# Performance work log

Measured on AMD Instinct MI355X. Metric: run time of the kernel, lower is better.

The kernel has to match this reference:

```python
import jax, jax.numpy as jnp
import numpy as np

DIM = 768
NUM_HEADS = 12
HEAD_DIM = DIM // NUM_HEADS
SCALE = HEAD_DIM ** -0.5


def setup_inputs() -> dict:
    key = jax.random.key(0)
    ks = jax.random.split(key, 6)
    B, N, C = 4, 2048, DIM
    x = jax.random.normal(ks[0], (B, N, C), dtype=jnp.float32)
    qkv_weight = jax.random.normal(ks[1], (3 * C, C), dtype=jnp.float32) * (C ** -0.5)
    q_bias = jax.random.normal(ks[2], (C,), dtype=jnp.float32) * 0.02
    v_bias = jax.random.normal(ks[3], (C,), dtype=jnp.float32) * 0.02
    proj_weight = jax.random.normal(ks[4], (C, C), dtype=jnp.float32) * (C ** -0.5)
    proj_bias = jax.random.normal(ks[5], (C,), dtype=jnp.float32) * 0.02
    return {"x": x, "qkv_weight": qkv_weight, "q_bias": q_bias,
            "v_bias": v_bias, "proj_weight": proj_weight, "proj_bias": proj_bias}


def reference(x, qkv_weight, q_bias, v_bias, proj_weight, proj_bias):
    B, N, C = x.shape
    # bias = concat(q_bias, zeros_like(v_bias), v_bias)
    bias = jnp.concatenate([q_bias, jnp.zeros_like(v_bias), v_bias])
    qkv = x @ qkv_weight.T + bias                      # [B, N, 3C]
    qkv = qkv.reshape(B, N, 3, NUM_HEADS, HEAD_DIM)
    q, k, v = jnp.moveaxis(qkv, 2, 0)                  # each [B, N, H, hd]
    q = jnp.transpose(q, (0, 2, 1, 3)) * SCALE         # [B, H, N, hd]
    k = jnp.transpose(k, (0, 2, 1, 3))
    v = jnp.transpose(v, (0, 2, 1, 3))
    attn = jax.nn.softmax(jnp.einsum('bhqd,bhkd->bhqk', q, k), axis=-1)
    out = jnp.einsum('bhqk,bhkd->bhqd', attn, v)       # [B, H, N, hd]
    out = jnp.transpose(out, (0, 2, 1, 3)).reshape(B, N, C)
    return out @ proj_weight.T + proj_bias
```

## Files before the change

kernel.cpp:

```cpp
#include <hip/hip_runtime.h>
#include <cstdint>
#include <cstddef>

typedef _Float16 f16;
typedef _Float16 f16x8 __attribute__((ext_vector_type(8)));
typedef _Float16 f16x4 __attribute__((ext_vector_type(4)));
typedef __fp16 h16x2 __attribute__((ext_vector_type(2)));
typedef float f32x4 __attribute__((ext_vector_type(4)));

#define DIM 768
#define NHEAD 12
#define HD 64
#define BATCH 4
#define SEQ 2048
#define MROWS (BATCH*SEQ)
#define C3 (3*DIM)
#define NBH (BATCH*NHEAD)

__device__ __forceinline__ f32x4 mfma32(f16x8 a, f16x8 b, f32x4 c) {
  return __builtin_amdgcn_mfma_f32_16x16x32_f16(a, b, c, 0, 0, 0);
}
__device__ __forceinline__ f32x4 mfma16(f16x4 a, f16x4 b, f32x4 c) {
  return __builtin_amdgcn_mfma_f32_16x16x16f16(a, b, c, 0, 0, 0);
}

__device__ __forceinline__ void gl2lds16(const void* g, void* l) {
  __builtin_amdgcn_global_load_lds(
      (const __attribute__((address_space(1))) void*)g,
      (__attribute__((address_space(3))) void*)l, 16, 0, 0);
}

__global__ __launch_bounds__(256) void k_convert(
    const float* __restrict__ x, const float* __restrict__ wqkv,
    const float* __restrict__ wproj,
    f16* __restrict__ xh, f16* __restrict__ wqh, f16* __restrict__ wph)
{
  const int NX = MROWS*DIM/4, NW = C3*DIM/4;
  int i = blockIdx.x * 256 + threadIdx.x;
  const float4* src; f16* dst; int idx;
  if (i < NX)         { src = (const float4*)x;     dst = xh;  idx = i; }
  else if (i < NX+NW) { src = (const float4*)wqkv;  dst = wqh; idx = i - NX; }
  else                { src = (const float4*)wproj; dst = wph; idx = i - NX - NW; }
  float4 v = src[idx];
  union { f16 h[4]; uint64_t u; } r;
  r.h[0] = (f16)v.x; r.h[1] = (f16)v.y; r.h[2] = (f16)v.z; r.h[3] = (f16)v.w;
  ((uint64_t*)dst)[idx] = r.u;
}

__device__ __forceinline__ void gemm_tile(
    const f16* __restrict__ A, const f16* __restrict__ B,
    int lda, int ldb, int K, int am0, int bn0,
    f16* smem, f32x4 acc[4][4])
{
  f16* sA0 = smem;         f16* sA1 = smem + 4096;
  f16* sB0 = smem + 8192;  f16* sB1 = smem + 12288;
  const int tid = threadIdx.x, wid = tid >> 6;
  const int lane = tid & 63, lane15 = lane & 15, quad = lane >> 4;
  const int wm = wid >> 1, wn = wid & 1;

  auto stage = [&](int k0, f16* sA, f16* sB) {
    #pragma unroll
    for (int i = 0; i < 2; i++) {
      int j = i*256 + tid;
      int row = j >> 2;
      int sc  = (j & 3) ^ ((row >> 1) & 3);
      gl2lds16(A + (size_t)(am0 + row)*lda + k0 + sc*8, sA + (i*256 + wid*64)*8);
      gl2lds16(B + (size_t)(bn0 + row)*ldb + k0 + sc*8, sB + (i*256 + wid*64)*8);
    }
  };

  const int NK = K >> 5;
  stage(0, sA0, sB0);
  for (int kk = 0; kk < NK; kk++) {
    f16* cA = (kk & 1) ? sA1 : sA0;
    f16* cB = (kk & 1) ? sB1 : sB0;
    __syncthreads();
    if (kk + 1 < NK)
      stage((kk + 1) << 5, (kk & 1) ? sA0 : sA1, (kk & 1) ? sB0 : sB1);
    f16x8 af[4], bf[4];
    #pragma unroll
    for (int t = 0; t < 4; t++) {
      int ra = wm*64 + t*16 + lane15;
      af[t] = *(const f16x8*)(cA + ra*32 + ((quad ^ ((ra >> 1) & 3)) << 3));
      int rb = wn*64 + t*16 + lane15;
      bf[t] = *(const f16x8*)(cB + rb*32 + ((quad ^ ((rb >> 1) & 3)) << 3));
    }
    #pragma unroll
    for (int mt = 0; mt < 4; mt++)
      #pragma unroll
      for (int nt = 0; nt < 4; nt++)
        acc[mt][nt] = mfma32(af[mt], bf[nt], acc[mt][nt]);
  }
}

__global__ __launch_bounds__(256, 4) void k_qkv(
    const f16* __restrict__ xh, const f16* __restrict__ wqh,
    const float* __restrict__ q_bias, const float* __restrict__ v_bias,
    f16* __restrict__ Qh, f16* __restrict__ Kh, f16* __restrict__ Vt)
{
  __shared__ f16 smem[16384];
  f32x4 acc[4][4];
  const f32x4 z4 = {0.f, 0.f, 0.f, 0.f};
  #pragma unroll
  for (int a = 0; a < 4; a++)
    #pragma unroll
    for (int b = 0; b < 4; b++) acc[a][b] = z4;

  const int tid = threadIdx.x, wid = tid >> 6, lane = tid & 63;
  const int lane15 = lane & 15, quad = lane >> 4;
  const int wm = wid >> 1, wn = wid & 1;
  const int cblk = blockIdx.x * 128;
  const int mblk = blockIdx.y * 128;
  const int bb = mblk >> 11, nbase = mblk & (SEQ - 1);
  const float QS = 0.125f * 1.4426950408889634f;

  if (cblk < 2*DIM) {
    gemm_tile(wqh, xh, DIM, DIM, DIM, cblk, mblk, smem, acc);
    const bool isQ = (cblk < DIM);
    #pragma unroll
    for (int mt = 0; mt < 4; mt++) {
      int c0 = cblk + wm*64 + mt*16 + quad*4;
      int cr = isQ ? c0 : (c0 - DIM);
      int h = cr >> 6, d0 = cr & 63;
      float4 qb4 = isQ ? *(const float4*)(q_bias + c0) : make_float4(0,0,0,0);
      f16* dst = isQ ? Qh : Kh;
      f16* base = dst + (((size_t)(bb*NHEAD + h)*SEQ + nbase) << 6) + d0;
      #pragma unroll
      for (int nt = 0; nt < 4; nt++) {
        int n = wn*64 + nt*16 + lane15;
        f32x4 v = acc[mt][nt];
        f16x4 hv;
        if (isQ) {
          hv[0] = (f16)((v[0] + qb4.x) * QS); hv[1] = (f16)((v[1] + qb4.y) * QS);
          hv[2] = (f16)((v[2] + qb4.z) * QS); hv[3] = (f16)((v[3] + qb4.w) * QS);
        } else {
          hv[0] = (f16)v[0]; hv[1] = (f16)v[1]; hv[2] = (f16)v[2]; hv[3] = (f16)v[3];
        }
        *(f16x4*)(base + ((size_t)n << 6)) = hv;
      }
    }
  } else {
    gemm_tile(xh, wqh, DIM, DIM, DIM, mblk, cblk, smem, acc);
    #pragma unroll
    for (int nt = 0; nt < 4; nt++) {
      int c = cblk + wn*64 + nt*16 + lane15;
      int c2 = c - 2*DIM;
      int h = c2 >> 6, d = c2 & 63;
      float b = v_bias[c2];
      f16* base = Vt + ((size_t)(bb*NHEAD + h)*HD + d)*SEQ + nbase;
      #pragma unroll
      for (int mt = 0; mt < 4; mt++) {
        int n0 = wm*64 + mt*16 + quad*4;
        f32x4 v = acc[mt][nt];
        f16x4 hv = {(f16)(v[0]+b), (f16)(v[1]+b), (f16)(v[2]+b), (f16)(v[3]+b)};
        *(f16x4*)(base + n0) = hv;
      }
    }
  }
}

#define KVT 128
#define NIT (SEQ/KVT)
__global__ __launch_bounds__(256, 3) void k_attn(
    const f16* __restrict__ Qh, const f16* __restrict__ Kh,
    const f16* __restrict__ Vt, f16* __restrict__ attnh)
{
  __shared__ f16 smem[2*8192 + 64*132];
  f16* sK0 = smem;
  f16* sK1 = smem + 8192;
  f16* sV  = smem + 16384;

  const int tid = threadIdx.x, wid = tid >> 6, lane = tid & 63;
  const int lane15 = lane & 15, quad = lane >> 4;
  const int q0 = blockIdx.x * 128;
  const int bh = blockIdx.y;
  const int qw = q0 + wid*32;

  const f16* Kbh = Kh + (size_t)bh*SEQ*HD;
  const f16* Vbh = Vt + (size_t)bh*HD*SEQ;

  f16x8 qf[2][2];
  #pragma unroll
  for (int qt = 0; qt < 2; qt++)
    #pragma unroll
    for (int ks = 0; ks < 2; ks++)
      qf[qt][ks] = *(const f16x8*)(Qh + ((size_t)bh*SEQ + qw + qt*16 + lane15)*HD
                                      + ks*32 + quad*8);

  f32x4 o[4][2];
  f32x4 sacc[2];
  const f32x4 z4 = {0.f, 0.f, 0.f, 0.f};
  #pragma unroll
  for (int dt = 0; dt < 4; dt++)
    #pragma unroll
    for (int qt = 0; qt < 2; qt++) o[dt][qt] = z4;
  sacc[0] = z4; sacc[1] = z4;
  const f16x4 one4 = {(f16)1.f, (f16)1.f, (f16)1.f, (f16)1.f};

  const int vrow = tid >> 2, vcg = (tid & 3) * 32;
  const f16* vsrc = Vbh + (size_t)vrow*SEQ + vcg;

  auto stageK = [&](int kv0, f16* sK) {
    #pragma unroll
    for (int i = 0; i < 4; i++) {
      int j = i*256 + tid;
      int row = j >> 3;
      int sc  = (j & 7) ^ (row & 7);
      gl2lds16(Kbh + (size_t)(kv0 + row)*HD + sc*8, sK + (i*256 + wid*64)*8);
    }
  };

  stageK(0, sK0);
  f16x8 vreg[4];
  #pragma unroll
  for (int j = 0; j < 4; j++) vreg[j] = *(const f16x8*)(vsrc + j*8);

  for (int it = 0; it < NIT; it++) {
    f16* cK = (it & 1) ? sK1 : sK0;
    __syncthreads();
    #pragma unroll
    for (int j = 0; j < 4; j++) {
      union { f16x8 v; f16x4 h[2]; } u; u.v = vreg[j];
      *(f16x4*)(sV + vrow*132 + vcg + j*8)     = u.h[0];
      *(f16x4*)(sV + vrow*132 + vcg + j*8 + 4) = u.h[1];
    }
    __syncthreads();
    if (it + 1 < NIT) {
      stageK((it + 1)*KVT, (it & 1) ? sK0 : sK1);
      #pragma unroll
      for (int j = 0; j < 4; j++)
        vreg[j] = *(const f16x8*)(vsrc + (it + 1)*KVT + j*8);
    }

    #pragma unroll
    for (int c = 0; c < 4; c++) {
      f16x8 ka[2][2];
      #pragma unroll
      for (int kt = 0; kt < 2; kt++) {
        int rb = c*32 + kt*16 + lane15;
        #pragma unroll
        for (int ks = 0; ks < 2; ks++)
          ka[ks][kt] = *(const f16x8*)(cK + rb*64 + (((ks*4 + quad) ^ (rb & 7)) << 3));
      }
      f32x4 s[2][2];
      #pragma unroll
      for (int kt = 0; kt < 2; kt++)
        #pragma unroll
        for (int qt = 0; qt < 2; qt++) s[kt][qt] = z4;
      #pragma unroll
      for (int ks = 0; ks < 2; ks++)
        #pragma unroll
        for (int kt = 0; kt < 2; kt++)
          #pragma unroll
          for (int qt = 0; qt < 2; qt++)
            s[kt][qt] = mfma32(ka[ks][kt], qf[qt][ks], s[kt][qt]);

      f16x4 pb[2][2];
      #pragma unroll
      for (int kt = 0; kt < 2; kt++)
        #pragma unroll
        for (int qt = 0; qt < 2; qt++) {
          union { h16x2 g2[2]; f16x4 h4; } u;
          u.g2[0] = __builtin_amdgcn_cvt_pkrtz(exp2f(s[kt][qt][0]), exp2f(s[kt][qt][1]));
          u.g2[1] = __builtin_amdgcn_cvt_pkrtz(exp2f(s[kt][qt][2]), exp2f(s[kt][qt][3]));
          pb[kt][qt] = u.h4;
        }
      #pragma unroll
      for (int kt = 0; kt < 2; kt++)
        #pragma unroll
        for (int qt = 0; qt < 2; qt++)
          sacc[qt] = mfma16(one4, pb[kt][qt], sacc[qt]);

      #pragma unroll
      for (int dt = 0; dt < 4; dt++) {
        int row = dt*16 + lane15;
        #pragma unroll
        for (int kt = 0; kt < 2; kt++) {
          int c16 = 4*c + 2*kt + (quad >> 1);
          f16x4 va = *(const f16x4*)(sV + row*132 + c16*8 + (quad & 1)*4);
          #pragma unroll
          for (int qt = 0; qt < 2; qt++)
            o[dt][qt] = mfma16(va, pb[kt][qt], o[dt][qt]);
        }
      }
    }
  }

  float inv[2] = {1.f / sacc[0][0], 1.f / sacc[1][0]};

  __syncthreads();
  f16* tb = smem + wid * (32 * 72);
  #pragma unroll
  for (int dt = 0; dt < 4; dt++)
    #pragma unroll
    for (int qt = 0; qt < 2; qt++) {
      f32x4 v = o[dt][qt];
      float iv = inv[qt];
      f16x4 hx = {(f16)(v[0]*iv), (f16)(v[1]*iv), (f16)(v[2]*iv), (f16)(v[3]*iv)};
      *(f16x4*)(tb + (qt*16 + lane15)*72 + dt*16 + quad*4) = hx;
    }
  __syncthreads();
  const int b = bh / NHEAD, h = bh % NHEAD;
  #pragma unroll
  for (int i = 0; i < 4; i++) {
    int row = i*8 + (lane >> 3);
    f16x8 rv = *(const f16x8*)(tb + row*72 + (lane & 7)*8);
    *(f16x8*)(attnh + ((size_t)b*SEQ + qw + row)*DIM + h*HD + (lane & 7)*8) = rv;
  }
}

__global__ __launch_bounds__(256, 4) void k_proj(
    const f16* __restrict__ ah, const f16* __restrict__ wph,
    const float* __restrict__ pbias, float* __restrict__ out)
{
  __shared__ f16 smem[16384];
  f32x4 acc[4][4];
  const f32x4 z4 = {0.f, 0.f, 0.f, 0.f};
  #pragma unroll
  for (int a = 0; a < 4; a++)
    #pragma unroll
    for (int b = 0; b < 4; b++) acc[a][b] = z4;

  const int cblk = blockIdx.y * 128;
  const int mblk = blockIdx.x * 128;
  gemm_tile(wph, ah, DIM, DIM, DIM, cblk, mblk, smem, acc);

  const int tid = threadIdx.x, wid = tid >> 6, lane = tid & 63;
  const int lane15 = lane & 15, quad = lane >> 4;
  const int wm = wid >> 1, wn = wid & 1;
  #pragma unroll
  for (int mt = 0; mt < 4; mt++) {
    int c0 = cblk + wm*64 + mt*16 + quad*4;
    float4 b4 = *(const float4*)(pbias + c0);
    #pragma unroll
    for (int nt = 0; nt < 4; nt++) {
      int m = mblk + wn*64 + nt*16 + lane15;
      f32x4 v = acc[mt][nt];
      float4 r = make_float4(v[0]+b4.x, v[1]+b4.y, v[2]+b4.z, v[3]+b4.w);
      *(float4*)(out + (size_t)m*DIM + c0) = r;
    }
  }
}

extern "C" void kernel_launch(void* const* d_in, const int* in_sizes, int n_in,
                              void* d_out, int out_size, void* d_ws, size_t ws_size,
                              hipStream_t stream) {
  const float* x    = (const float*)d_in[0];
  const float* wqkv = (const float*)d_in[1];
  const float* qb   = (const float*)d_in[2];
  const float* vb   = (const float*)d_in[3];
  const float* wp   = (const float*)d_in[4];
  const float* pb   = (const float*)d_in[5];
  float* out = (float*)d_out;

  f16* p = (f16*)d_ws;
  f16* xh  = p; p += (size_t)MROWS*DIM;
  f16* wqh = p; p += (size_t)C3*DIM;
  f16* wph = p; p += (size_t)DIM*DIM;
  f16* Qh  = p; p += (size_t)NBH*SEQ*HD;
  f16* Kh  = p; p += (size_t)NBH*SEQ*HD;
  f16* Vt  = p; p += (size_t)NBH*SEQ*HD;
  f16* attnh = xh;

  k_convert<<<8448, 256, 0, stream>>>(x, wqkv, wp, xh, wqh, wph);
  k_qkv<<<dim3(C3/128, MROWS/128), 256, 0, stream>>>(xh, wqh, qb, vb, Qh, Kh, Vt);
  k_attn<<<dim3(SEQ/128, NBH), 256, 0, stream>>>(Qh, Kh, Vt, attnh);
  k_proj<<<dim3(MROWS/128, DIM/128), 256, 0, stream>>>(attnh, wph, pb, out);
}
```

Before: 236.4 us.

## Use 32x32x16 MFMA in attention, read V directly from global, remap blocks per XCD

The attention kernel moves from 16x16 MFMA tiles to 32x32x16 MFMA, so each wave computes a 32x32 score tile with fewer, larger instructions. The probabilities are rearranged across lanes with ds_bpermute so they can be fed as the B operand of the PV product. V is no longer staged in LDS: each lane loads its V fragments straight from global memory, which removes one barrier per iteration and the LDS writes. The grid is flattened and remapped so that all blocks of one batch-head land on the same XCD, improving L2 reuse of K/V. The trade-offs are exposed global-load latency for V inside the inner loop and extra bpermute traffic.

```diff
diff --git a/kernel.cpp b/kernel.cpp
--- a/kernel.cpp
+++ b/kernel.cpp
@@ -7,6 +7,7 @@
 typedef _Float16 f16x4 __attribute__((ext_vector_type(4)));
 typedef __fp16 h16x2 __attribute__((ext_vector_type(2)));
 typedef float f32x4 __attribute__((ext_vector_type(4)));
+typedef float f32x16 __attribute__((ext_vector_type(16)));
 
 #define DIM 768
 #define NHEAD 12
@@ -20,8 +21,8 @@
 __device__ __forceinline__ f32x4 mfma32(f16x8 a, f16x8 b, f32x4 c) {
   return __builtin_amdgcn_mfma_f32_16x16x32_f16(a, b, c, 0, 0, 0);
 }
-__device__ __forceinline__ f32x4 mfma16(f16x4 a, f16x4 b, f32x4 c) {
-  return __builtin_amdgcn_mfma_f32_16x16x16f16(a, b, c, 0, 0, 0);
+__device__ __forceinline__ f32x16 mfma3232(f16x8 a, f16x8 b, f32x16 c) {
+  return __builtin_amdgcn_mfma_f32_32x32x16_f16(a, b, c, 0, 0, 0);
 }
 
 __device__ __forceinline__ void gl2lds16(const void* g, void* l) {
@@ -165,40 +166,33 @@
     const f16* __restrict__ Qh, const f16* __restrict__ Kh,
     const f16* __restrict__ Vt, f16* __restrict__ attnh)
 {
-  __shared__ f16 smem[2*8192 + 64*132];
+  __shared__ f16 smem[16384];
   f16* sK0 = smem;
   f16* sK1 = smem + 8192;
-  f16* sV  = smem + 16384;
 
   const int tid = threadIdx.x, wid = tid >> 6, lane = tid & 63;
-  const int lane15 = lane & 15, quad = lane >> 4;
-  const int q0 = blockIdx.x * 128;
-  const int bh = blockIdx.y;
+  const int l31 = lane & 31, hi = lane >> 5;
+
+  const int L = blockIdx.x;
+  const int xcd = L & 7, kk = L >> 3;
+  const int bh = xcd + 8*(kk >> 4);
+  const int q0 = (kk & 15) * 128;
   const int qw = q0 + wid*32;
 
   const f16* Kbh = Kh + (size_t)bh*SEQ*HD;
   const f16* Vbh = Vt + (size_t)bh*HD*SEQ;
 
-  f16x8 qf[2][2];
-  #pragma unroll
-  for (int qt = 0; qt < 2; qt++)
-    #pragma unroll
-    for (int ks = 0; ks < 2; ks++)
-      qf[qt][ks] = *(const f16x8*)(Qh + ((size_t)bh*SEQ + qw + qt*16 + lane15)*HD
-                                      + ks*32 + quad*8);
-
-  f32x4 o[4][2];
-  f32x4 sacc[2];
-  const f32x4 z4 = {0.f, 0.f, 0.f, 0.f};
-  #pragma unroll
-  for (int dt = 0; dt < 4; dt++)
-    #pragma unroll
-    for (int qt = 0; qt < 2; qt++) o[dt][qt] = z4;
-  sacc[0] = z4; sacc[1] = z4;
-  const f16x4 one4 = {(f16)1.f, (f16)1.f, (f16)1.f, (f16)1.f};
-
-  const int vrow = tid >> 2, vcg = (tid & 3) * 32;
-  const f16* vsrc = Vbh + (size_t)vrow*SEQ + vcg;
+  f16x8 qf[4];
+  #pragma unroll
+  for (int ks = 0; ks < 4; ks++)
+    qf[ks] = *(const f16x8*)(Qh + ((size_t)bh*SEQ + qw + l31)*HD + ks*16 + hi*8);
+
+  const f32x16 z16 = {0.f,0.f,0.f,0.f, 0.f,0.f,0.f,0.f,
+                      0.f,0.f,0.f,0.f, 0.f,0.f,0.f,0.f};
+  f32x16 o0 = z16, o1 = z16, sacc = z16;
+  f16x8 one8;
+  #pragma unroll
+  for (int j = 0; j < 8; j++) one8[j] = (f16)1.f;
 
   auto stageK = [&](int kv0, f16* sK) {
     #pragma unroll
@@ -210,102 +204,93 @@
     }
   };
 
+  int koff[4];
+  #pragma unroll
+  for (int ks = 0; ks < 4; ks++)
+    koff[ks] = l31*64 + (((2*ks + hi) ^ (l31 & 7)) << 3);
+
+  const f16* vb0 = Vbh + (size_t)l31*SEQ + hi*8;
+  const f16* vb1 = Vbh + (size_t)(32 + l31)*SEQ + hi*8;
+
+  const int pidx = (lane ^ 32) << 2;
+
   stageK(0, sK0);
-  f16x8 vreg[4];
-  #pragma unroll
-  for (int j = 0; j < 4; j++) vreg[j] = *(const f16x8*)(vsrc + j*8);
 
   for (int it = 0; it < NIT; it++) {
     f16* cK = (it & 1) ? sK1 : sK0;
     __syncthreads();
-    #pragma unroll
-    for (int j = 0; j < 4; j++) {
-      union { f16x8 v; f16x4 h[2]; } u; u.v = vreg[j];
-      *(f16x4*)(sV + vrow*132 + vcg + j*8)     = u.h[0];
-      *(f16x4*)(sV + vrow*132 + vcg + j*8 + 4) = u.h[1];
-    }
-    __syncthreads();
-    if (it + 1 < NIT) {
+    if (it + 1 < NIT)
       stageK((it + 1)*KVT, (it & 1) ? sK0 : sK1);
-      #pragma unroll
-      for (int j = 0; j < 4; j++)
-        vreg[j] = *(const f16x8*)(vsrc + (it + 1)*KVT + j*8);
-    }
 
     #pragma unroll
     for (int c = 0; c < 4; c++) {
-      f16x8 ka[2][2];
-      #pragma unroll
-      for (int kt = 0; kt < 2; kt++) {
-        int rb = c*32 + kt*16 + lane15;
-        #pragma unroll
-        for (int ks = 0; ks < 2; ks++)
-          ka[ks][kt] = *(const f16x8*)(cK + rb*64 + (((ks*4 + quad) ^ (rb & 7)) << 3));
+      const int p = it*KVT + c*32;
+      f16x8 va00 = *(const f16x8*)(vb0 + p);
+      f16x8 va01 = *(const f16x8*)(vb0 + p + 16);
+      f16x8 va10 = *(const f16x8*)(vb1 + p);
+      f16x8 va11 = *(const f16x8*)(vb1 + p + 16);
+
+      f32x16 s = z16;
+      #pragma unroll
+      for (int ks = 0; ks < 4; ks++) {
+        f16x8 ka = *(const f16x8*)(cK + c*2048 + koff[ks]);
+        s = mfma3232(ka, qf[ks], s);
       }
-      f32x4 s[2][2];
-      #pragma unroll
-      for (int kt = 0; kt < 2; kt++)
-        #pragma unroll
-        for (int qt = 0; qt < 2; qt++) s[kt][qt] = z4;
-      #pragma unroll
-      for (int ks = 0; ks < 2; ks++)
-        #pragma unroll
-        for (int kt = 0; kt < 2; kt++)
-          #pragma unroll
-          for (int qt = 0; qt < 2; qt++)
-            s[kt][qt] = mfma32(ka[ks][kt], qf[qt][ks], s[kt][qt]);
-
-      f16x4 pb[2][2];
-      #pragma unroll
-      for (int kt = 0; kt < 2; kt++)
-        #pragma unroll
-        for (int qt = 0; qt < 2; qt++) {
-          union { h16x2 g2[2]; f16x4 h4; } u;
-          u.g2[0] = __builtin_amdgcn_cvt_pkrtz(exp2f(s[kt][qt][0]), exp2f(s[kt][qt][1]));
-          u.g2[1] = __builtin_amdgcn_cvt_pkrtz(exp2f(s[kt][qt][2]), exp2f(s[kt][qt][3]));
-          pb[kt][qt] = u.h4;
-        }
-      #pragma unroll
-      for (int kt = 0; kt < 2; kt++)
-        #pragma unroll
-        for (int qt = 0; qt < 2; qt++)
-          sacc[qt] = mfma16(one4, pb[kt][qt], sacc[qt]);
-
-      #pragma unroll
-      for (int dt = 0; dt < 4; dt++) {
-        int row = dt*16 + lane15;
-        #pragma unroll
-        for (int kt = 0; kt < 2; kt++) {
-          int c16 = 4*c + 2*kt + (quad >> 1);
-          f16x4 va = *(const f16x4*)(sV + row*132 + c16*8 + (quad & 1)*4);
-          #pragma unroll
-          for (int qt = 0; qt < 2; qt++)
-            o[dt][qt] = mfma16(va, pb[kt][qt], o[dt][qt]);
-        }
+
+      unsigned h[8];
+      #pragma unroll
+      for (int r = 0; r < 8; r++) {
+        union { h16x2 p2; unsigned u; } uu;
+        uu.p2 = __builtin_amdgcn_cvt_pkrtz(exp2f(s[2*r]), exp2f(s[2*r+1]));
+        h[r] = uu.u;
       }
-    }
-  }
-
-  float inv[2] = {1.f / sacc[0][0], 1.f / sacc[1][0]};
+      int X0 = __builtin_amdgcn_ds_bpermute(pidx, (int)h[0]);
+      int X1 = __builtin_amdgcn_ds_bpermute(pidx, (int)h[1]);
+      int X2 = __builtin_amdgcn_ds_bpermute(pidx, (int)h[2]);
+      int X3 = __builtin_amdgcn_ds_bpermute(pidx, (int)h[3]);
+      int X4 = __builtin_amdgcn_ds_bpermute(pidx, (int)h[4]);
+      int X5 = __builtin_amdgcn_ds_bpermute(pidx, (int)h[5]);
+      int X6 = __builtin_amdgcn_ds_bpermute(pidx, (int)h[6]);
+      int X7 = __builtin_amdgcn_ds_bpermute(pidx, (int)h[7]);
+      union { unsigned w[4]; f16x8 v; } b0u, b1u;
+      b0u.w[0] = hi ? (unsigned)X2 : h[0];
+      b0u.w[1] = hi ? (unsigned)X3 : h[1];
+      b0u.w[2] = hi ? h[2] : (unsigned)X0;
+      b0u.w[3] = hi ? h[3] : (unsigned)X1;
+      b1u.w[0] = hi ? (unsigned)X6 : h[4];
+      b1u.w[1] = hi ? (unsigned)X7 : h[5];
+      b1u.w[2] = hi ? h[6] : (unsigned)X4;
+      b1u.w[3] = hi ? h[7] : (unsigned)X5;
+
+      sacc = mfma3232(one8, b0u.v, sacc);
+      sacc = mfma3232(one8, b1u.v, sacc);
+      o0 = mfma3232(va00, b0u.v, o0);
+      o0 = mfma3232(va01, b1u.v, o0);
+      o1 = mfma3232(va10, b0u.v, o1);
+      o1 = mfma3232(va11, b1u.v, o1);
+    }
+  }
+
+  const float inv = 1.f / sacc[0];
 
   __syncthreads();
   f16* tb = smem + wid * (32 * 72);
   #pragma unroll
-  for (int dt = 0; dt < 4; dt++)
-    #pragma unroll
-    for (int qt = 0; qt < 2; qt++) {
-      f32x4 v = o[dt][qt];
-      float iv = inv[qt];
-      f16x4 hx = {(f16)(v[0]*iv), (f16)(v[1]*iv), (f16)(v[2]*iv), (f16)(v[3]*iv)};
-      *(f16x4*)(tb + (qt*16 + lane15)*72 + dt*16 + quad*4) = hx;
-    }
+  for (int g = 0; g < 4; g++) {
+    f16x4 h0v = {(f16)(o0[4*g+0]*inv), (f16)(o0[4*g+1]*inv),
+                 (f16)(o0[4*g+2]*inv), (f16)(o0[4*g+3]*inv)};
+    *(f16x4*)(tb + l31*72 + g*8 + hi*4) = h0v;
+    f16x4 h1v = {(f16)(o1[4*g+0]*inv), (f16)(o1[4*g+1]*inv),
+                 (f16)(o1[4*g+2]*inv), (f16)(o1[4*g+3]*inv)};
+    *(f16x4*)(tb + l31*72 + 32 + g*8 + hi*4) = h1v;
+  }
   __syncthreads();
-  const int b = bh / NHEAD, h = bh % NHEAD;
+  const int b = bh / NHEAD, hh = bh % NHEAD;
   #pragma unroll
   for (int i = 0; i < 4; i++) {
     int row = i*8 + (lane >> 3);
     f16x8 rv = *(const f16x8*)(tb + row*72 + (lane & 7)*8);
-    *(f16x8*)(attnh + ((size_t)b*SEQ + qw + row)*DIM + h*HD + (lane & 7)*8) = rv;
+    *(f16x8*)(attnh + ((size_t)b*SEQ + qw + row)*DIM + hh*HD + (lane & 7)*8) = rv;
   }
 }
 
@@ -364,6 +349,6 @@
 
   k_convert<<<8448, 256, 0, stream>>>(x, wqkv, wp, xh, wqh, wph);
   k_qkv<<<dim3(C3/128, MROWS/128), 256, 0, stream>>>(xh, wqh, qb, vb, Qh, Kh, Vt);
-  k_attn<<<dim3(SEQ/128, NBH), 256, 0, stream>>>(Qh, Kh, Vt, attnh);
+  k_attn<<<dim3((SEQ/128)*NBH), 256, 0, stream>>>(Qh, Kh, Vt, attnh);
   k_proj<<<dim3(MROWS/128, DIM/128), 256, 0, stream>>>(attnh, wph, pb, out);
 }
```

Result: slower. 251.0 us (+6.2%).
